# Kernel tuning notes

Hardware: AMD Instinct MI355X
Metric: run time of the kernel (lower is better)

The kernel has to match this reference:

```python
import jax, jax.numpy as jnp
import numpy as np

QMAX8 = 127.0  # 2**(8-1)-1


def quant1(x, scale):
    # 1-bit symmetric quant: s * sign(x), s = |scale| (per-group mean scale)
    return jnp.abs(scale) * jnp.sign(x)


def quant8(x, scale):
    s = jnp.maximum(jnp.abs(scale), 1e-8)
    q = jnp.clip(jnp.round(x / s), -QMAX8, QMAX8)
    return q * s


def setup_inputs() -> dict:
    key = jax.random.key(0)
    ks = jax.random.split(key, 5)
    p, j, k, m, l, n = 2, 32, 32, 32, 8, 32
    x = jax.random.normal(ks[0], (2, 1024, k * n), dtype=jnp.float32)
    Y_fp = jax.random.normal(ks[1], (p, j, k, m, l), dtype=jnp.float32)
    Z_fp = jax.random.normal(ks[2], (p, j, k, l, n), dtype=jnp.float32)
    A = jax.random.normal(ks[3], (p, j, k, 4), dtype=jnp.float32)
    bias = jax.random.normal(ks[4], (j * m,), dtype=jnp.float32)
    act_scale = jnp.full((1,), 0.001, dtype=jnp.float32)
    return {"x": x, "Y_fp": Y_fp, "Z_fp": Z_fp, "A": A, "bias": bias,
            "act_scale": act_scale}


def reference(x, Y_fp, Z_fp, A, bias, act_scale):
    p, j, k, m, l = Y_fp.shape
    n = Z_fp.shape[-1]
    orig_shape = x.shape[:-1]
    X = x.astype(jnp.float32)
    X = quant8(X, act_scale)  # activation quantization (act_bits=8)

    # per-(p,j,k) mean-abs scales over last two dims
    Y_scale = jnp.mean(jnp.abs(Y_fp), axis=(-2, -1), keepdims=True)
    Z_scale = jnp.mean(jnp.abs(Z_fp), axis=(-2, -1), keepdims=True)
    Y_q = quant1(Y_fp, Y_scale)  # (p,j,k,m,l)
    Z_q = quant1(Z_fp, Z_scale)  # (p,j,k,l,n)

    X_kn = X.reshape(-1, k, n)  # (B,k,n)
    T = jnp.einsum('bkn,pjkln->bpjkl', X_kn, Z_q)
    core = jnp.einsum('pjkml,bpjkl->bpjkm', Y_q, T)

    # quant_bias=True correction terms
    a = A[..., 0][None, ..., None]            # (1,p,j,k,1)
    out1 = jnp.sum(core * a, axis=(1, 3))     # (B,j,m)
    Y_sum = jnp.sum(Y_q, axis=-1)             # (p,j,k,m)
    B_coef = jnp.sum(A[..., 1][..., None] * Y_sum, axis=0)  # (j,k,m)
    Sx = jnp.sum(X_kn, axis=-1)               # (B,k)
    out2 = jnp.einsum('bk,jkm->bjm', Sx, B_coef)
    Zs = jnp.sum(Z_q, axis=-2)                # (p,j,k,n)
    Tz = jnp.einsum('bkn,pjkn->bpjk', X_kn, Zs)
    out3 = jnp.sum(Tz * A[..., 2][None], axis=(1, 3))[..., None]  # (B,j,1)
    D_coef = jnp.sum(A[..., 3], axis=0)       # (j,k)
    out4 = jnp.einsum('bk,jk->bj', Sx, D_coef)[..., None]          # (B,j,1)

    out_bjm = out1 + out2 + out3 + out4       # (B,j,m) via broadcast
    out_2d = out_bjm.reshape(-1, j * m) + bias
    out = out_2d.reshape(*orig_shape, j * m)
    return out.astype(x.dtype)
```

## Files before the change

### kernel.cpp

```cpp
#include <hip/hip_runtime.h>
#include <math.h>
#include <stdint.h>


typedef __attribute__((ext_vector_type(8))) short bf16x8;
typedef __attribute__((ext_vector_type(4))) float f32x4;
typedef __attribute__((ext_vector_type(4))) unsigned short us4;

__device__ __forceinline__ unsigned short f2bf(float f) {
    union { float f; uint32_t u; } c; c.f = f;
    uint32_t r = 0x7fffu + ((c.u >> 16) & 1u);
    return (unsigned short)((c.u + r) >> 16);
}

__device__ __forceinline__ void gl2lds16(const void* g, void* l) {
    __builtin_amdgcn_global_load_lds(
        (const __attribute__((address_space(1))) void*)g,
        (__attribute__((address_space(3))) void*)l, 16, 0, 0);
}

__global__ __launch_bounds__(256) void fused_pre(
    const float* __restrict__ Y,
    const float* __restrict__ Z,
    const float* __restrict__ A,
    const float* __restrict__ x,
    const float* __restrict__ act_scale,
    unsigned short* __restrict__ wt,
    unsigned short* __restrict__ qx)
{
    const int t = threadIdx.x;

    if (blockIdx.x >= 1024) {
        const float s = fmaxf(fabsf(act_scale[0]), 1e-8f);
        const int b2 = blockIdx.x - 1024;
        #pragma unroll
        for (int it = 0; it < 4; ++it) {
            const size_t i4 = (size_t)b2 * 256 + t + (size_t)it * 131072;
            const float4 v = *(const float4*)(x + i4 * 4);
            us4 o;
            o.x = f2bf(fminf(fmaxf(rintf(v.x / s), -127.f), 127.f));
            o.y = f2bf(fminf(fmaxf(rintf(v.y / s), -127.f), 127.f));
            o.z = f2bf(fminf(fmaxf(rintf(v.z / s), -127.f), 127.f));
            o.w = f2bf(fminf(fmaxf(rintf(v.w / s), -127.f), 127.f));
            *(us4*)(qx + i4 * 4) = o;
        }
        return;
    }

    __shared__ unsigned int yb[2][8];
    __shared__ unsigned int zb[2][8];
    __shared__ float wred[16];

    const int jk = blockIdx.x;
    const int jj = jk >> 5;
    const int kk = jk & 31;
    const int n  = t & 31;
    const int mb = t >> 5;
    const int w  = t >> 6;
    const int lane = t & 63;

    const int base0 = jj * 32 + kk;
    const int base1 = 1024 + base0;

    const float yv0 = Y[(size_t)base0 * 256 + t];
    const float yv1 = Y[(size_t)base1 * 256 + t];
    const float zv0 = Z[(size_t)base0 * 256 + t];
    const float zv1 = Z[(size_t)base1 * 256 + t];
    const float a00 = A[(size_t)base0 * 4 + 0], a01 = A[(size_t)base0 * 4 + 1];
    const float a02 = A[(size_t)base0 * 4 + 2], a03 = A[(size_t)base0 * 4 + 3];
    const float a10 = A[(size_t)base1 * 4 + 0], a11 = A[(size_t)base1 * 4 + 1];
    const float a12 = A[(size_t)base1 * 4 + 2], a13 = A[(size_t)base1 * 4 + 3];

    const unsigned long long by0 = __ballot(yv0 < 0.f);
    const unsigned long long by1 = __ballot(yv1 < 0.f);
    const unsigned long long bz0 = __ballot(zv0 < 0.f);
    const unsigned long long bz1 = __ballot(zv1 < 0.f);
    if (lane == 0) {
        yb[0][2 * w] = (unsigned)by0; yb[0][2 * w + 1] = (unsigned)(by0 >> 32);
        yb[1][2 * w] = (unsigned)by1; yb[1][2 * w + 1] = (unsigned)(by1 >> 32);
        zb[0][2 * w] = (unsigned)bz0; zb[0][2 * w + 1] = (unsigned)(bz0 >> 32);
        zb[1][2 * w] = (unsigned)bz1; zb[1][2 * w + 1] = (unsigned)(bz1 >> 32);
    }

    float ay0 = fabsf(yv0), az0 = fabsf(zv0);
    float ay1 = fabsf(yv1), az1 = fabsf(zv1);
    #pragma unroll
    for (int d = 1; d < 64; d <<= 1) {
        ay0 += __shfl_xor(ay0, d, 64);
        az0 += __shfl_xor(az0, d, 64);
        ay1 += __shfl_xor(ay1, d, 64);
        az1 += __shfl_xor(az1, d, 64);
    }
    if (lane == 0) {
        wred[w * 4 + 0] = ay0;
        wred[w * 4 + 1] = az0;
        wred[w * 4 + 2] = ay1;
        wred[w * 4 + 3] = az1;
    }
    __syncthreads();

    const float sY0 = (wred[0] + wred[4] + wred[8]  + wred[12]) * (1.f / 256.f);
    const float sZ0 = (wred[1] + wred[5] + wred[9]  + wred[13]) * (1.f / 256.f);
    const float sY1 = (wred[2] + wred[6] + wred[10] + wred[14]) * (1.f / 256.f);
    const float sZ1 = (wred[3] + wred[7] + wred[11] + wred[15]) * (1.f / 256.f);

    const float c00 = a00 * sY0 * sZ0, c01 = a01 * sY0, c02 = a02 * sZ0;
    const float c10 = a10 * sY1 * sZ1, c11 = a11 * sY1, c12 = a12 * sZ1;
    const float cb  = a03 + a13;

    unsigned sz0 = 0, sz1 = 0;
    #pragma unroll
    for (int l = 0; l < 8; ++l) {
        sz0 |= ((zb[0][l] >> n) & 1u) << l;
        sz1 |= ((zb[1][l] >> n) & 1u) << l;
    }
    const float zc0 = 8.f - 2.f * (float)__popc(sz0);
    const float zc1 = 8.f - 2.f * (float)__popc(sz1);
    const float czc = c02 * zc0 + c12 * zc1 + cb;

    const int ybw = (mb >> 2);
    const int ybs = (mb & 3) * 8;

    #pragma unroll
    for (int q = 0; q < 4; ++q) {
        const int m = mb + 8 * q;
        const unsigned sy0 = (yb[0][2 * q + ybw] >> ybs) & 0xffu;
        const unsigned sy1 = (yb[1][2 * q + ybw] >> ybs) & 0xffu;
        const float w0  = 8.f - 2.f * (float)__popc(sy0 ^ sz0);
        const float w1  = 8.f - 2.f * (float)__popc(sy1 ^ sz1);
        const float ys0 = 8.f - 2.f * (float)__popc(sy0);
        const float ys1 = 8.f - 2.f * (float)__popc(sy1);
        const float acc = c00 * w0 + c01 * ys0 + c10 * w1 + c11 * ys1 + czc;
        wt[(size_t)(jj * 32 + m) * 1024 + kk * 32 + n] = f2bf(acc);
    }
}

__global__ __launch_bounds__(256) void gemm_mfma(
    const unsigned short* __restrict__ qx,
    const unsigned short* __restrict__ wt,
    const float* __restrict__ bias,
    const float* __restrict__ act_scale,
    float* __restrict__ out)
{
    __shared__ __align__(16) short lds[2 * 8192];

    const int tid  = threadIdx.x;
    const int lane = tid & 63;
    const int wave = tid >> 6;
    const int wm = wave >> 1;
    const int wn = wave & 1;
    const int rowBase = blockIdx.y * 64;
    const int colBase = blockIdx.x * 64;

    const float s = fmaxf(fabsf(act_scale[0]), 1e-8f);

    f32x4 acc[2][2];
    #pragma unroll
    for (int i = 0; i < 2; ++i)
        #pragma unroll
        for (int jx = 0; jx < 2; ++jx)
            acc[i][jx] = (f32x4)0.f;

    const int lr = lane >> 3;
    const int kx = (lane & 7) ^ lr;
    const unsigned short* ag[2];
    const unsigned short* bg[2];
    #pragma unroll
    for (int i = 0; i < 2; ++i) {
        const int g = i * 4 + wave;
        ag[i] = qx + (size_t)(rowBase + g * 8 + lr) * 1024 + kx * 8;
        bg[i] = wt + (size_t)(colBase + g * 8 + lr) * 1024 + kx * 8;
    }

    char* const ldsc = (char*)lds;
    const int q4  = lane >> 4;
    const int l16 = lane & 15;

    #pragma unroll
    for (int i = 0; i < 2; ++i) {
        const int g = i * 4 + wave;
        gl2lds16(ag[i], ldsc + g * 1024);
        gl2lds16(bg[i], ldsc + 8192 + g * 1024);
    }

    for (int kt = 0; kt < 16; ++kt) {
        __syncthreads();

        if (kt + 1 < 16) {
            const int k1 = (kt + 1) * 64;
            char* bb = ldsc + ((kt + 1) & 1) * 16384;
            #pragma unroll
            for (int i = 0; i < 2; ++i) {
                const int g = i * 4 + wave;
                gl2lds16(ag[i] + k1, bb + g * 1024);
                gl2lds16(bg[i] + k1, bb + 8192 + g * 1024);
            }
        }

        const short* As = lds + (kt & 1) * 8192;
        const short* Bs = As + 4096;

        #pragma unroll
        for (int kk2 = 0; kk2 < 2; ++kk2) {
            const int kc = kk2 * 4 + q4;
            bf16x8 af[2], bfr[2];
            #pragma unroll
            for (int im = 0; im < 2; ++im) {
                const int r = wm * 32 + im * 16 + l16;
                af[im] = *(const bf16x8*)&As[(r * 8 + (kc ^ (r & 7))) * 8];
            }
            #pragma unroll
            for (int in = 0; in < 2; ++in) {
                const int r = wn * 32 + in * 16 + l16;
                bfr[in] = *(const bf16x8*)&Bs[(r * 8 + (kc ^ (r & 7))) * 8];
            }
            #pragma unroll
            for (int im = 0; im < 2; ++im)
                #pragma unroll
                for (int in = 0; in < 2; ++in)
                    acc[im][in] = __builtin_amdgcn_mfma_f32_16x16x32_bf16(
                        af[im], bfr[in], acc[im][in], 0, 0, 0);
        }
    }

    #pragma unroll
    for (int im = 0; im < 2; ++im) {
        #pragma unroll
        for (int in = 0; in < 2; ++in) {
            const int col = colBase + wn * 32 + in * 16 + l16;
            const float b = bias[col];
            #pragma unroll
            for (int r = 0; r < 4; ++r) {
                const int row = rowBase + wm * 32 + im * 16 + q4 * 4 + r;
                out[(size_t)row * 1024 + col] = s * acc[im][in][r] + b;
            }
        }
    }
}

extern "C" void kernel_launch(void* const* d_in, const int* in_sizes, int n_in,
                              void* d_out, int out_size, void* d_ws, size_t ws_size,
                              hipStream_t stream) {
    const float* x         = (const float*)d_in[0];
    const float* Y_fp      = (const float*)d_in[1];
    const float* Z_fp      = (const float*)d_in[2];
    const float* A         = (const float*)d_in[3];
    const float* bias      = (const float*)d_in[4];
    const float* act_scale = (const float*)d_in[5];
    float* out = (float*)d_out;

    unsigned short* wtp = (unsigned short*)d_ws;
    unsigned short* qxp = (unsigned short*)((char*)d_ws + 2 * 1024 * 1024);

    fused_pre<<<dim3(1536), dim3(256), 0, stream>>>(Y_fp, Z_fp, A, x, act_scale, wtp, qxp);
    gemm_mfma<<<dim3(16, 32), dim3(256), 0, stream>>>(qxp, wtp, bias, act_scale, out);
}
```

Before: 82.69 us.

## Replace LDS double-buffered GEMM with direct global-to-register MFMA operand loads

The GEMM kernel drops the shared-memory staging (global_load_lds into double-buffered swizzled LDS tiles plus per-iteration barriers). Each wave now loads its bf16 MFMA fragments straight from global memory into registers, with the K loop unrolled by four. This removes the barrier and LDS traffic, but operands are no longer shared across waves in a block, so every wave re-reads them through the cache. Each lane also issues 16-byte loads strided by rows, which may coalesce less well.

```diff
diff --git a/kernel.cpp b/kernel.cpp
--- a/kernel.cpp
+++ b/kernel.cpp
@@ -11,12 +11,6 @@
     union { float f; uint32_t u; } c; c.f = f;
     uint32_t r = 0x7fffu + ((c.u >> 16) & 1u);
     return (unsigned short)((c.u + r) >> 16);
-}
-
-__device__ __forceinline__ void gl2lds16(const void* g, void* l) {
-    __builtin_amdgcn_global_load_lds(
-        (const __attribute__((address_space(1))) void*)g,
-        (__attribute__((address_space(3))) void*)l, 16, 0, 0);
 }
 
 __global__ __launch_bounds__(256) void fused_pre(
@@ -135,15 +129,13 @@
     }
 }
 
-__global__ __launch_bounds__(256) void gemm_mfma(
+__global__ __launch_bounds__(256) void gemm_direct(
     const unsigned short* __restrict__ qx,
     const unsigned short* __restrict__ wt,
     const float* __restrict__ bias,
     const float* __restrict__ act_scale,
     float* __restrict__ out)
 {
-    __shared__ __align__(16) short lds[2 * 8192];
-
     const int tid  = threadIdx.x;
     const int lane = tid & 63;
     const int wave = tid >> 6;
@@ -151,6 +143,8 @@
     const int wn = wave & 1;
     const int rowBase = blockIdx.y * 64;
     const int colBase = blockIdx.x * 64;
+    const int q4  = lane >> 4;
+    const int l16 = lane & 15;
 
     const float s = fmaxf(fabsf(act_scale[0]), 1e-8f);
 
@@ -161,66 +155,21 @@
         for (int jx = 0; jx < 2; ++jx)
             acc[i][jx] = (f32x4)0.f;
 
-    const int lr = lane >> 3;
-    const int kx = (lane & 7) ^ lr;
-    const unsigned short* ag[2];
-    const unsigned short* bg[2];
-    #pragma unroll
-    for (int i = 0; i < 2; ++i) {
-        const int g = i * 4 + wave;
-        ag[i] = qx + (size_t)(rowBase + g * 8 + lr) * 1024 + kx * 8;
-        bg[i] = wt + (size_t)(colBase + g * 8 + lr) * 1024 + kx * 8;
-    }
-
-    char* const ldsc = (char*)lds;
-    const int q4  = lane >> 4;
-    const int l16 = lane & 15;
-
-    #pragma unroll
-    for (int i = 0; i < 2; ++i) {
-        const int g = i * 4 + wave;
-        gl2lds16(ag[i], ldsc + g * 1024);
-        gl2lds16(bg[i], ldsc + 8192 + g * 1024);
-    }
-
-    for (int kt = 0; kt < 16; ++kt) {
-        __syncthreads();
-
-        if (kt + 1 < 16) {
-            const int k1 = (kt + 1) * 64;
-            char* bb = ldsc + ((kt + 1) & 1) * 16384;
-            #pragma unroll
-            for (int i = 0; i < 2; ++i) {
-                const int g = i * 4 + wave;
-                gl2lds16(ag[i] + k1, bb + g * 1024);
-                gl2lds16(bg[i] + k1, bb + 8192 + g * 1024);
-            }
-        }
-
-        const short* As = lds + (kt & 1) * 8192;
-        const short* Bs = As + 4096;
-
-        #pragma unroll
-        for (int kk2 = 0; kk2 < 2; ++kk2) {
-            const int kc = kk2 * 4 + q4;
-            bf16x8 af[2], bfr[2];
-            #pragma unroll
-            for (int im = 0; im < 2; ++im) {
-                const int r = wm * 32 + im * 16 + l16;
-                af[im] = *(const bf16x8*)&As[(r * 8 + (kc ^ (r & 7))) * 8];
-            }
-            #pragma unroll
-            for (int in = 0; in < 2; ++in) {
-                const int r = wn * 32 + in * 16 + l16;
-                bfr[in] = *(const bf16x8*)&Bs[(r * 8 + (kc ^ (r & 7))) * 8];
-            }
-            #pragma unroll
-            for (int im = 0; im < 2; ++im)
-                #pragma unroll
-                for (int in = 0; in < 2; ++in)
-                    acc[im][in] = __builtin_amdgcn_mfma_f32_16x16x32_bf16(
-                        af[im], bfr[in], acc[im][in], 0, 0, 0);
-        }
+    const unsigned short* a0 = qx + (size_t)(rowBase + wm * 32 + l16)      * 1024 + q4 * 8;
+    const unsigned short* a1 = qx + (size_t)(rowBase + wm * 32 + 16 + l16) * 1024 + q4 * 8;
+    const unsigned short* b0 = wt + (size_t)(colBase + wn * 32 + l16)      * 1024 + q4 * 8;
+    const unsigned short* b1 = wt + (size_t)(colBase + wn * 32 + 16 + l16) * 1024 + q4 * 8;
+
+    #pragma unroll 4
+    for (int k0 = 0; k0 < 1024; k0 += 32) {
+        const bf16x8 af0 = *(const bf16x8*)(a0 + k0);
+        const bf16x8 af1 = *(const bf16x8*)(a1 + k0);
+        const bf16x8 bf0 = *(const bf16x8*)(b0 + k0);
+        const bf16x8 bf1 = *(const bf16x8*)(b1 + k0);
+        acc[0][0] = __builtin_amdgcn_mfma_f32_16x16x32_bf16(af0, bf0, acc[0][0], 0, 0, 0);
+        acc[0][1] = __builtin_amdgcn_mfma_f32_16x16x32_bf16(af0, bf1, acc[0][1], 0, 0, 0);
+        acc[1][0] = __builtin_amdgcn_mfma_f32_16x16x32_bf16(af1, bf0, acc[1][0], 0, 0, 0);
+        acc[1][1] = __builtin_amdgcn_mfma_f32_16x16x32_bf16(af1, bf1, acc[1][1], 0, 0, 0);
     }
 
     #pragma unroll
@@ -253,5 +202,5 @@
     unsigned short* qxp = (unsigned short*)((char*)d_ws + 2 * 1024 * 1024);
 
     fused_pre<<<dim3(1536), dim3(256), 0, stream>>>(Y_fp, Z_fp, A, x, act_scale, wtp, qxp);
-    gemm_mfma<<<dim3(16, 32), dim3(256), 0, stream>>>(qxp, wtp, bias, act_scale, out);
-}
+    gemm_direct<<<dim3(16, 32), dim3(256), 0, stream>>>(qxp, wtp, bias, act_scale, out);
+}
```

Measured after the change: 104.3 us. 26.2% more time.
